# Performance work log

Measured on AMD Instinct MI355X. Metric: run time of the kernel, lower is better.

Reference implementation:

```python
import jax, jax.numpy as jnp
import numpy as np

NUM = 8          # group_heads
ALPHA = 1000.0   # Pos_Enc alpha
BETA = 100.0     # Pos_Enc beta


def setup_inputs() -> dict:
    key = jax.random.key(0)
    ks = jax.random.split(key, 19)
    N, C, H = 16384, 64, 1024
    gs1 = H // NUM
    s = 0.02
    r = lambda k, shp: jax.random.normal(k, shp, dtype=jnp.float32) * s
    return {
        "features": jax.random.normal(ks[0], (N, C), dtype=jnp.float32),
        "fc1_w": r(ks[1], (C, H)), "fc1_b": r(ks[2], (H,)),
        "fc2_w": r(ks[3], (H, C)), "fc2_b": r(ks[4], (C,)),
        "g1_w": r(ks[5], (H, H)), "g1_b": r(ks[6], (H,)),
        "g2_w": r(ks[7], (H, H)), "g2_b": r(ks[8], (H,)),
        "gg1_w": r(ks[9], (gs1, gs1)), "gg1_b": r(ks[10], (gs1,)),
        "gg2_w": r(ks[11], (gs1, gs1)), "gg2_b": r(ks[12], (gs1,)),
        "wq": r(ks[13], (H, H)), "wk": r(ks[14], (H, H)), "wv": r(ks[15], (H, H)),
        "wq2": r(ks[16], (gs1, gs1)), "wk2": r(ks[17], (gs1, gs1)),
        "lpe": jax.random.normal(ks[18], (1,), dtype=jnp.float32) * 0.1,
    }


def _mlp(x, w1, b1, w2, b2):
    return jax.nn.relu(x @ w1 + b1) @ w2 + b2


def reference(features, fc1_w, fc1_b, fc2_w, fc2_b, g1_w, g1_b, g2_w, g2_b,
              gg1_w, gg1_b, gg2_w, gg2_b, wq, wk, wv, wq2, wk2, lpe):
    N, C = features.shape
    H = fc1_w.shape[1]
    gs1 = H // NUM   # feature-group size
    gs2 = N // NUM   # token-group size

    x = features @ fc1_w + fc1_b                      # (N, H)

    # --- attn1: per-feature-group vector attention (shared weights -> vectorized)
    xg = x.reshape(N, NUM, gs1)                       # contiguous feature slices
    q1 = xg @ wq2
    k1 = xg @ wk2
    h1 = _mlp(q1 - k1, gg1_w, gg1_b, gg2_w, gg2_b)
    attn1 = jax.nn.softmax(h1 / np.sqrt(gs1).astype(np.float32), axis=0)
    attn1 = attn1.reshape(N, H)                       # concat over groups = reshape

    # --- attn2: source bug: loop uses stale i=NUM-1, so the LAST token group
    # is processed NUM times and tiled along tokens.
    gf2 = x[(NUM - 1) * gs2:, :]                      # (gs2, H)
    q2 = gf2 @ wq
    k2 = gf2 @ wk
    h2 = _mlp(q2 - k2, g1_w, g1_b, g2_w, g2_b)
    a2 = jax.nn.softmax(h2 / np.sqrt(H).astype(np.float32), axis=0)
    attn2 = jnp.tile(a2, (NUM, 1))                    # (N, H)

    attn = attn1 + attn2
    v = x @ wv                                        # (N, H)

    # --- sinusoidal positional encoding (Pos_Enc), only coord-0 slice survives
    xyz = features[:, :3]                             # (N, 3)
    feat_dim = H // 2
    feat_range = jnp.arange(feat_dim, dtype=jnp.float32)
    dim_embed = jnp.power(jnp.float32(ALPHA), feat_range / feat_dim)
    div = BETA * xyz[..., None] / dim_embed           # (N, 3, feat_dim)
    emb = jnp.concatenate([jnp.sin(div), jnp.cos(div)], axis=-1)  # (N, 3, H)
    pe = (emb + lpe[0]) * lpe[0]
    pe0 = pe[:, 0, :]                                 # (N, H) first coordinate

    res = attn * (v + pe0)                            # elementwise einsum bmf,bmf->bmf
    out = res @ fc2_w + fc2_b + features              # residual
    return out
```

## Files before the change

### kernel.cpp

```cpp
#include <hip/hip_runtime.h>
#include <hip/hip_bf16.h>
#include <math.h>
#include <type_traits>


typedef __attribute__((ext_vector_type(8))) short short8;
typedef __attribute__((ext_vector_type(4))) float f32x4;
typedef __attribute__((ext_vector_type(4))) float float4v;

#define GLOAD_LDS16(gptr, lptr)                                                 \
    __builtin_amdgcn_global_load_lds(                                           \
        (const __attribute__((address_space(1))) void*)(gptr),                  \
        (__attribute__((address_space(3))) void*)(lptr), 16, 0, 0)

static __device__ __forceinline__ unsigned short f2bf_bits(float v) {
    __hip_bfloat16 h = __float2bfloat16(v);
    return __builtin_bit_cast(unsigned short, h);
}
static __device__ __forceinline__ float bf_bits2f(unsigned short u) {
    return __bfloat162float(__builtin_bit_cast(__hip_bfloat16, u));
}
static __device__ __forceinline__ int swz16(int r, int c16) {
    return (r << 4) + (c16 ^ (r & 7));
}
static __device__ __forceinline__ int swz_elem(int r, int c) {
    return (r << 7) + ((((c << 1) ^ ((r & 7) << 4))) >> 1);
}
static __device__ __forceinline__ int xcd_swz(int bid, int nwg) {
    return (bid & 7) * (nwg >> 3) + (bid >> 3);
}

static __device__ void conv_t_dev(const float* __restrict__ A, const float* __restrict__ Bsub,
                                  __hip_bfloat16* __restrict__ Ot, int K, int N,
                                  int bx, int by, int tid, float* t )
{
    const int n0 = bx * 32, k0 = by * 128;
    const int tx = tid & 31, ty = tid >> 5;
    const int ksub = (K - k0 < 128) ? (K - k0) / 32 : 4;
    for (int s = 0; s < ksub; ++s) {
        const int kk = k0 + s * 32;
        #pragma unroll
        for (int j = 0; j < 4; ++j) {
            int k = kk + ty + j * 8;
            float v = A[(long)k * N + n0 + tx];
            if (Bsub) v -= Bsub[(long)k * N + n0 + tx];
            t[(ty + j * 8) * 33 + tx] = v;
        }
        __syncthreads();
        #pragma unroll
        for (int j = 0; j < 4; ++j) {
            int n = n0 + ty + j * 8;
            Ot[(long)n * K + kk + tx] = __float2bfloat16(t[tx * 33 + ty + j * 8]);
        }
        __syncthreads();
    }
}

__global__ __launch_bounds__(256) void prep_k(
    const float* __restrict__ features, const float* __restrict__ fc2_w,
    const float* __restrict__ fc2_b, const float* __restrict__ g1_w,
    const float* __restrict__ g2_w, const float* __restrict__ wq,
    const float* __restrict__ wk, const float* __restrict__ wv,
    const float* __restrict__ wq2, const float* __restrict__ wk2,
    const float* __restrict__ gg1_w, const float* __restrict__ gg2_w,
    __hip_bfloat16* __restrict__ fc2T, __hip_bfloat16* __restrict__ wdT,
    __hip_bfloat16* __restrict__ wvT, __hip_bfloat16* __restrict__ g1T,
    __hip_bfloat16* __restrict__ g2T, __hip_bfloat16* __restrict__ wd2T,
    __hip_bfloat16* __restrict__ gg1T, __hip_bfloat16* __restrict__ gg2T,
    float* __restrict__ invde, float* __restrict__ out)
{
    __shared__ float t[32 * 33];
    const int bid = blockIdx.x;
    const int tid = threadIdx.x;

    if (bid == 0) {
        #pragma unroll
        for (int i = 0; i < 2; ++i) {
            int idx = tid + i * 256;
            invde[idx] = exp2f(-9.96578428466209f * (float)idx * (1.f / 512.f));
        }
    } else if (bid < 257) {
        const float4v* f4 = (const float4v*)features;
        float4v* o4 = (float4v*)out;
        const float4v* b4 = (const float4v*)fc2_b;
        long base = (long)(bid - 1) * 1024;
        #pragma unroll
        for (int i = 0; i < 4; ++i) {
            long idx = base + tid + i * 256;
            o4[idx] = f4[idx] + b4[idx & 15];
        }
    } else if (bid < 513) {
        int tt = bid - 257;  conv_t_dev(wq, wk, wdT, 1024, 1024, tt & 31, tt >> 5, tid, t);
    } else if (bid < 769) {
        int tt = bid - 513;  conv_t_dev(wv, nullptr, wvT, 1024, 1024, tt & 31, tt >> 5, tid, t);
    } else if (bid < 1025) {
        int tt = bid - 769;  conv_t_dev(g1_w, nullptr, g1T, 1024, 1024, tt & 31, tt >> 5, tid, t);
    } else if (bid < 1281) {
        int tt = bid - 1025; conv_t_dev(g2_w, nullptr, g2T, 1024, 1024, tt & 31, tt >> 5, tid, t);
    } else if (bid < 1297) {
        int tt = bid - 1281; conv_t_dev(fc2_w, nullptr, fc2T, 1024, 64, tt & 1, tt >> 1, tid, t);
    } else if (bid < 1301) {
        int tt = bid - 1297; conv_t_dev(wq2, wk2, wd2T, 128, 128, tt & 3, 0, tid, t);
    } else if (bid < 1305) {
        int tt = bid - 1301; conv_t_dev(gg1_w, nullptr, gg1T, 128, 128, tt & 3, 0, tid, t);
    } else {
        int tt = bid - 1305; conv_t_dev(gg2_w, nullptr, gg2T, 128, 128, tt & 3, 0, tid, t);
    }
}

__global__ __launch_bounds__(256) void xgemm_k(
    const float* __restrict__ features, const float* __restrict__ fc1_w,
    const float* __restrict__ fc1_b, __hip_bfloat16* __restrict__ xb)
{
    __shared__ __align__(16) char smem[32768];
    unsigned short* As = (unsigned short*)smem;
    unsigned short* Bs = (unsigned short*)(smem + 16384);
    const int tile = blockIdx.x;
    const int tid = threadIdx.x;
    const int bm = (tile >> 3) << 7, bn = (tile & 7) << 7;
    const int wid = tid >> 6, lane = tid & 63;
    const int wm = (wid >> 1) << 6, wn = (wid & 1) << 6;
    const int l15 = lane & 15, kg = lane >> 4;

    #pragma unroll
    for (int i = 0; i < 8; ++i) {
        int idx = i * 256 + tid;
        int r = idx >> 4, c4 = idx & 15;
        float4v f = *(const float4v*)(features + (long)(bm + r) * 64 + c4 * 4);
        unsigned int p0 = f2bf_bits(f[0]) | ((unsigned int)f2bf_bits(f[1]) << 16);
        unsigned int p1 = f2bf_bits(f[2]) | ((unsigned int)f2bf_bits(f[3]) << 16);
        int dst = r * 64 + (((c4 >> 1) ^ (r & 7)) << 3) + (c4 & 1) * 4;
        unsigned int* p = (unsigned int*)&As[dst];
        p[0] = p0; p[1] = p1;
    }
    #pragma unroll
    for (int i = 0; i < 8; ++i) {
        int idx = i * 256 + tid;
        int k = idx >> 5, c4b = idx & 31;
        float4v g = *(const float4v*)(fc1_w + (long)k * 1024 + bn + c4b * 4);
        #pragma unroll
        for (int q = 0; q < 4; ++q) {
            int n = c4b * 4 + q;
            Bs[n * 64 + (((k >> 3) ^ (n & 7)) << 3) + (k & 7)] = f2bf_bits(g[q]);
        }
    }
    __syncthreads();

    f32x4 acc[4][4] = {};
    #pragma unroll
    for (int ks2 = 0; ks2 < 2; ++ks2) {
        const int kslot = ks2 * 4 + kg;
        short8 af[4], bf_[4];
        #pragma unroll
        for (int m = 0; m < 4; ++m) {
            int r = wm + m * 16 + l15;
            af[m] = *(const short8*)&As[r * 64 + ((kslot ^ (r & 7)) << 3)];
        }
        #pragma unroll
        for (int n = 0; n < 4; ++n) {
            int r = wn + n * 16 + l15;
            bf_[n] = *(const short8*)&Bs[r * 64 + ((kslot ^ (r & 7)) << 3)];
        }
        #pragma unroll
        for (int m = 0; m < 4; ++m)
            #pragma unroll
            for (int n = 0; n < 4; ++n)
                acc[m][n] = __builtin_amdgcn_mfma_f32_16x16x32_bf16(
                    af[m], bf_[n], acc[m][n], 0, 0, 0);
    }
    const int rq = kg << 2;
    #pragma unroll
    for (int n = 0; n < 4; ++n) {
        const int col = bn + wn + n * 16 + l15;
        const float bv = fc1_b[col];
        #pragma unroll
        for (int m = 0; m < 4; ++m)
            #pragma unroll
            for (int j = 0; j < 4; ++j)
                xb[(long)(bm + wm + m * 16 + rq + j) * 1024 + col] =
                    __float2bfloat16(acc[m][n][j] + bv);
    }
}

template <int OP, bool CS>
static __device__ void gemm6464_dev(
    const __hip_bfloat16* __restrict__ A, const __hip_bfloat16* __restrict__ Bt,
    const float* __restrict__ bias, __hip_bfloat16* __restrict__ Co,
    float scale, float* __restrict__ pcs, int swz, int tid, char* smem)
{
    const int wid = tid >> 6, lane = tid & 63;
    const int bm = (swz >> 4) << 6, bn = (swz & 15) << 6;
    const int wm = (wid >> 1) << 5, wn = (wid & 1) << 5;
    f32x4 acc[2][2] = {};
    const int l15 = lane & 15, kg = lane >> 4;
    const int rS = tid >> 2;
    const int c4s = (tid & 3) ^ ((rS >> 1) & 3);

#define G66_STAGE(b, k0)                                                        \
    { char* base = smem + (b) * 8192;                                           \
      GLOAD_LDS16(A + (long)(bm + rS) * 1024 + (k0) + c4s * 8,                  \
                  base + (wid << 6) * 16);                                      \
      GLOAD_LDS16(Bt + (long)(bn + rS) * 1024 + (k0) + c4s * 8,                 \
                  base + 4096 + (wid << 6) * 16); }

    G66_STAGE(0, 0);
    #pragma unroll 2
    for (int kt = 0; kt < 32; ++kt) {
        if (kt < 31) {
            G66_STAGE((kt + 1) & 1, (kt + 1) * 32);
            asm volatile("s_waitcnt vmcnt(2)" ::: "memory");
        } else {
            asm volatile("s_waitcnt vmcnt(0)" ::: "memory");
        }
        __builtin_amdgcn_s_barrier();
        __builtin_amdgcn_sched_barrier(0);
        const char* AsB = smem + (kt & 1) * 8192;
        const char* BsB = AsB + 4096;
        short8 af[2], bf_[2];
        #pragma unroll
        for (int m = 0; m < 2; ++m) {
            const int R = wm + m * 16 + l15;
            af[m] = *(const short8*)(AsB + R * 64 + ((kg ^ ((R >> 1) & 3)) << 4));
        }
        #pragma unroll
        for (int n = 0; n < 2; ++n) {
            const int R = wn + n * 16 + l15;
            bf_[n] = *(const short8*)(BsB + R * 64 + ((kg ^ ((R >> 1) & 3)) << 4));
        }
        __builtin_amdgcn_s_setprio(1);
        #pragma unroll
        for (int m = 0; m < 2; ++m)
            #pragma unroll
            for (int n = 0; n < 2; ++n)
                acc[m][n] = __builtin_amdgcn_mfma_f32_16x16x32_bf16(
                    af[m], bf_[n], acc[m][n], 0, 0, 0);
        __builtin_amdgcn_s_setprio(0);
        __builtin_amdgcn_s_barrier();
    }
#undef G66_STAGE

    const int rq = kg << 2;
    float csum[2];
    #pragma unroll
    for (int n = 0; n < 2; ++n) {
        const int col = bn + wn + n * 16 + l15;
        const float bv = bias ? bias[col] : 0.f;
        csum[n] = 0.f;
        #pragma unroll
        for (int m = 0; m < 2; ++m) {
            #pragma unroll
            for (int j = 0; j < 4; ++j) {
                const int row = bm + wm + m * 16 + rq + j;
                float cv = acc[m][n][j] + bv;
                if (OP == 1) cv = fmaxf(cv, 0.f);
                if (OP == 2) cv = __expf(cv * scale);
                if (CS) csum[n] += cv;
                Co[(long)row * 1024 + col] = __float2bfloat16(cv);
            }
        }
    }
    if (CS) {
        __syncthreads();
        float* ps = (float*)smem;
        const int slot = ((wid >> 1) << 2) | kg;
        #pragma unroll
        for (int n = 0; n < 2; ++n)
            ps[(wn + n * 16 + l15) * 8 + slot] = csum[n];
        __syncthreads();
        if (tid < 64) {
            float s = 0.f;
            #pragma unroll
            for (int q = 0; q < 8; ++q) s += ps[tid * 8 + q];
            pcs[(long)(swz >> 4) * 1024 + bn + tid] = s;
        }
    }
}

__global__ __launch_bounds__(256) void t1_k(
    const __hip_bfloat16* __restrict__ A, const __hip_bfloat16* __restrict__ Bt,
    __hip_bfloat16* __restrict__ Co)
{
    __shared__ __align__(16) char smem[16384];
    const int swz = xcd_swz(blockIdx.y * gridDim.x + blockIdx.x, gridDim.x * gridDim.y);
    gemm6464_dev<0, false>(A, Bt, nullptr, Co, 0.f, nullptr, swz, threadIdx.x, smem);
}
__global__ __launch_bounds__(256) void t2_k(
    const __hip_bfloat16* __restrict__ A, const __hip_bfloat16* __restrict__ Bt,
    const float* __restrict__ bias, __hip_bfloat16* __restrict__ Co)
{
    __shared__ __align__(16) char smem[16384];
    const int swz = xcd_swz(blockIdx.y * gridDim.x + blockIdx.x, gridDim.x * gridDim.y);
    gemm6464_dev<1, false>(A, Bt, bias, Co, 0.f, nullptr, swz, threadIdx.x, smem);
}
__global__ __launch_bounds__(256) void t3_k(
    const __hip_bfloat16* __restrict__ A, const __hip_bfloat16* __restrict__ Bt,
    const float* __restrict__ bias, __hip_bfloat16* __restrict__ Co,
    float* __restrict__ pcs)
{
    __shared__ __align__(16) char smem[16384];
    const int swz = xcd_swz(blockIdx.y * gridDim.x + blockIdx.x, gridDim.x * gridDim.y);
    gemm6464_dev<2, true>(A, Bt, bias, Co, 0.03125f, pcs, swz, threadIdx.x, smem);
}

__global__ __launch_bounds__(256) void chain_k(
    const __hip_bfloat16* __restrict__ xb,
    const __hip_bfloat16* __restrict__ w1T,
    const __hip_bfloat16* __restrict__ w2T,
    const __hip_bfloat16* __restrict__ w3T,
    const float* __restrict__ b2, const float* __restrict__ b3,
    __hip_bfloat16* __restrict__ e1, float* __restrict__ pcs1)
{
    __shared__ __align__(16) char smem[65536];
    unsigned short* act = (unsigned short*)smem;
    unsigned short* Wb  = (unsigned short*)(smem + 32768);
    const int tid = threadIdx.x;
    const int wid = tid >> 6, lane = tid & 63;
    const int wm = (wid >> 1) << 6, wn = (wid & 1) << 6;
    const int tileIdx = blockIdx.x;
    const long tile = (long)tileIdx * (128 * 128);

    #pragma unroll
    for (int i = 0; i < 8; ++i) {
        int L = i * 256 + wid * 64 + lane;
        int r = L >> 4, c16o = (L & 15) ^ (r & 7);
        GLOAD_LDS16(xb + tile + r * 128 + c16o * 8,
                    (char*)act + (i * 256 + wid * 64) * 16);
        GLOAD_LDS16(w1T + r * 128 + c16o * 8,
                    (char*)Wb + (i * 256 + wid * 64) * 16);
    }
    __syncthreads();

    f32x4 acc[4][4];
    const int rq = (lane >> 4) << 2;

#define CHAIN_ZERO()                                                            \
    _Pragma("unroll") for (int m = 0; m < 4; ++m)                               \
        _Pragma("unroll") for (int n = 0; n < 4; ++n)                           \
            acc[m][n] = (f32x4){0.f, 0.f, 0.f, 0.f};

#define CHAIN_MM()                                                              \
    _Pragma("unroll") for (int ks = 0; ks < 4; ++ks) {                          \
        short8 af[4], bfv[4];                                                   \
        const int kc = ks * 4 + (lane >> 4);                                    \
        _Pragma("unroll") for (int m = 0; m < 4; ++m) {                         \
            int r = wm + m * 16 + (lane & 15);                                  \
            af[m] = *(const short8*)((const char*)act + swz16(r, kc) * 16);     \
        }                                                                       \
        _Pragma("unroll") for (int n = 0; n < 4; ++n) {                         \
            int r = wn + n * 16 + (lane & 15);                                  \
            bfv[n] = *(const short8*)((const char*)Wb + swz16(r, kc) * 16);     \
        }                                                                       \
        _Pragma("unroll") for (int m = 0; m < 4; ++m)                           \
            _Pragma("unroll") for (int n = 0; n < 4; ++n)                       \
                acc[m][n] = __builtin_amdgcn_mfma_f32_16x16x32_bf16(            \
                    af[m], bfv[n], acc[m][n], 0, 0, 0);                         \
    }

#define STAGE_W(wptr)                                                           \
    _Pragma("unroll") for (int i = 0; i < 8; ++i) {                             \
        int L = i * 256 + wid * 64 + lane;                                      \
        int r = L >> 4, c16o = (L & 15) ^ (r & 7);                              \
        GLOAD_LDS16((wptr) + r * 128 + c16o * 8,                                \
                    (char*)Wb + (i * 256 + wid * 64) * 16);                     \
    }

    CHAIN_ZERO(); CHAIN_MM();
    __syncthreads();
    STAGE_W(w2T);
    #pragma unroll
    for (int m = 0; m < 4; ++m)
        #pragma unroll
        for (int n = 0; n < 4; ++n)
            #pragma unroll
            for (int j = 0; j < 4; ++j) {
                int row = wm + m * 16 + rq + j, col = wn + n * 16 + (lane & 15);
                act[swz_elem(row, col)] = f2bf_bits(acc[m][n][j]);
            }
    __syncthreads();

    CHAIN_ZERO(); CHAIN_MM();
    __syncthreads();
    STAGE_W(w3T);
    {
        float bv[4];
        #pragma unroll
        for (int n = 0; n < 4; ++n) bv[n] = b2[wn + n * 16 + (lane & 15)];
        #pragma unroll
        for (int m = 0; m < 4; ++m)
            #pragma unroll
            for (int n = 0; n < 4; ++n)
                #pragma unroll
                for (int j = 0; j < 4; ++j) {
                    int row = wm + m * 16 + rq + j, col = wn + n * 16 + (lane & 15);
                    act[swz_elem(row, col)] = f2bf_bits(fmaxf(acc[m][n][j] + bv[n], 0.f));
                }
    }
    __syncthreads();

    CHAIN_ZERO(); CHAIN_MM();
    __syncthreads();
    {
        float bv[4];
        #pragma unroll
        for (int n = 0; n < 4; ++n) bv[n] = b3[wn + n * 16 + (lane & 15)];
        #pragma unroll
        for (int m = 0; m < 4; ++m)
            #pragma unroll
            for (int n = 0; n < 4; ++n)
                #pragma unroll
                for (int j = 0; j < 4; ++j) {
                    int row = wm + m * 16 + rq + j, col = wn + n * 16 + (lane & 15);
                    float ev = __expf((acc[m][n][j] + bv[n]) * 0.08838834764831845f);
                    act[swz_elem(row, col)] = f2bf_bits(ev);
                }
    }
    __syncthreads();

    #pragma unroll
    for (int i = 0; i < 8; ++i) {
        int idx = i * 256 + tid;
        int r = idx >> 4, c16o = idx & 15;
        short8 vd = *(const short8*)((const char*)act + swz16(r, c16o) * 16);
        *(short8*)((__hip_bfloat16*)e1 + tile + r * 128 + c16o * 8) = vd;
    }
    #pragma unroll
    for (int i = 0; i < 4; ++i) {
        int p = i * 256 + tid;
        int g = p >> 7, c = p & 127;
        float s = 0.f;
        #pragma unroll
        for (int t16 = 0; t16 < 16; ++t16) {
            int r = t16 * 8 + g;
            s += bf_bits2f(act[swz_elem(r, c)]);
        }
        pcs1[(long)tileIdx * 1024 + p] = s;
    }
#undef CHAIN_ZERO
#undef CHAIN_MM
#undef STAGE_W
}

__global__ __launch_bounds__(1024) void reduce_k(
    const float* __restrict__ pcs1, const float* __restrict__ pcs2,
    float* __restrict__ rcs1, float* __restrict__ rcs2)
{
    __shared__ float red[16][64];
    const int tx = threadIdx.x, ty = threadIdx.y;
    if (blockIdx.x < 16) {
        const int col = blockIdx.x * 64 + tx;
        float s = 0.f;
        for (int p = ty; p < 1024; p += 16) s += pcs1[(long)p * 1024 + col];
        red[ty][tx] = s;
        __syncthreads();
        if (ty == 0) {
            float t = 0.f;
            #pragma unroll
            for (int q = 0; q < 16; ++q) t += red[q][tx];
            rcs1[col] = 1.f / t;
        }
    } else {
        const int col = (blockIdx.x - 16) * 64 + tx;
        float s = 0.f;
        for (int p = ty; p < 32; p += 16) s += pcs2[(long)p * 1024 + col];
        red[ty][tx] = s;
        __syncthreads();
        if (ty == 0) {
            float t = 0.f;
            #pragma unroll
            for (int q = 0; q < 16; ++q) t += red[q][tx];
            rcs2[col] = 1.f / t;
        }
    }
}

__global__ __launch_bounds__(256) void vres_k(
    const __hip_bfloat16* __restrict__ A, const __hip_bfloat16* __restrict__ Bt,
    const __hip_bfloat16* __restrict__ e1, const __hip_bfloat16* __restrict__ e2,
    const float* __restrict__ rcs1, const float* __restrict__ rcs2,
    const float* __restrict__ invde, const float* __restrict__ feats,
    const float* __restrict__ lpe, const __hip_bfloat16* __restrict__ fc2T,
    float* __restrict__ out)
{
    __shared__ __align__(16) char smem[65536];
    unsigned short* st = (unsigned short*)smem;

    const int tid = threadIdx.x;
    const int wid = tid >> 6;
    const int lane = tid & 63;
    const int swz = xcd_swz(blockIdx.y * gridDim.x + blockIdx.x, gridDim.x * gridDim.y);
    const int bm = (swz >> 3) << 7, bn = (swz & 7) << 7;
    const int wm = (wid >> 1) << 6, wn = (wid & 1) << 6;

    f32x4 acc[4][4] = {};
    const int c8 = tid & 7;
    const int l15 = lane & 15;
    const int kg = lane >> 4;
    const int arow = wm + l15;
    const int brow = wn + l15;

#define VR_STAGE(b, k0)                                                         \
    { char* base = smem + (b) * 32768;                                          \
      _Pragma("unroll") for (int i = 0; i < 4; ++i) {                           \
        const int r = i * 32 + (tid >> 3);                                      \
        const int c8s = c8 ^ (r & 7);                                           \
        GLOAD_LDS16(A + (long)(bm + r) * 1024 + (k0) + c8s * 8,                 \
                    base + (i * 256 + wid * 64) * 16);                          \
        GLOAD_LDS16(Bt + (long)(bn + r) * 1024 + (k0) + c8s * 8,                \
                    base + 16384 + (i * 256 + wid * 64) * 16); } }

    VR_STAGE(0, 0);
    #pragma unroll 2
    for (int kt = 0; kt < 16; ++kt) {
        if (kt < 15) {
            VR_STAGE((kt + 1) & 1, (kt + 1) * 64);
            asm volatile("s_waitcnt vmcnt(8)" ::: "memory");
        } else {
            asm volatile("s_waitcnt vmcnt(0)" ::: "memory");
        }
        __builtin_amdgcn_s_barrier();
        __builtin_amdgcn_sched_barrier(0);
        const __hip_bfloat16* As = (const __hip_bfloat16*)(smem + (kt & 1) * 32768);
        const __hip_bfloat16* Bs = (const __hip_bfloat16*)(smem + (kt & 1) * 32768 + 16384);
        __builtin_amdgcn_s_setprio(1);
        #pragma unroll
        for (int ks2 = 0; ks2 < 2; ++ks2) {
            const int kslot = ks2 * 4 + kg;
            short8 af[4], bf_[4];
            #pragma unroll
            for (int m = 0; m < 4; ++m) {
                const int r = arow + m * 16;
                af[m] = *(const short8*)(As + (r * 8 + (kslot ^ (r & 7))) * 8);
            }
            #pragma unroll
            for (int n = 0; n < 4; ++n) {
                const int r = brow + n * 16;
                bf_[n] = *(const short8*)(Bs + (r * 8 + (kslot ^ (r & 7))) * 8);
            }
            #pragma unroll
            for (int m = 0; m < 4; ++m)
                #pragma unroll
                for (int n = 0; n < 4; ++n)
                    acc[m][n] = __builtin_amdgcn_mfma_f32_16x16x32_bf16(
                        af[m], bf_[n], acc[m][n], 0, 0, 0);
        }
        __builtin_amdgcn_s_setprio(0);
        __builtin_amdgcn_s_barrier();
    }
#undef VR_STAGE

    const int rq = kg << 2;
    #pragma unroll
    for (int m = 0; m < 4; ++m)
        #pragma unroll
        for (int n = 0; n < 4; ++n)
            #pragma unroll
            for (int j = 0; j < 4; ++j)
                st[(wm + m * 16 + rq + j) * 136 + wn + n * 16 + l15] =
                    f2bf_bits(acc[m][n][j]);
    __syncthreads();

    const float lp = lpe[0];
    #pragma unroll
    for (int p = 0; p < 4; ++p) {
        const int r = p * 32 + (tid >> 3);
        const int cc = (tid & 7) << 4;
        const int grow = bm + r;
        const float angs = 100.f * feats[(long)grow * 64];
        const long goff = (long)grow * 1024 + bn + cc;
        const long goff2 = (long)(grow & 2047) * 1024 + bn + cc;
        short8 ev1[2], ev2[2], sv[2];
        ev1[0] = *(const short8*)((const unsigned short*)e1 + goff);
        ev1[1] = *(const short8*)((const unsigned short*)e1 + goff + 8);
        ev2[0] = *(const short8*)((const unsigned short*)e2 + goff2);
        ev2[1] = *(const short8*)((const unsigned short*)e2 + goff2 + 8);
        sv[0] = *(const short8*)&st[r * 136 + cc];
        sv[1] = *(const short8*)&st[r * 136 + cc + 8];
        unsigned short ov[16];
        #pragma unroll
        for (int q = 0; q < 16; ++q) {
            const int h = bn + cc + q;
            const float ang = angs * invde[h & 511];
            const float tr = (h < 512) ? __sinf(ang) : __cosf(ang);
            const float a = bf_bits2f((unsigned short)ev1[q >> 3][q & 7]) * rcs1[h] +
                            bf_bits2f((unsigned short)ev2[q >> 3][q & 7]) * rcs2[h];
            const float vv = bf_bits2f((unsigned short)sv[q >> 3][q & 7]);
            ov[q] = f2bf_bits(a * (vv + (tr + lp) * lp));
        }
        *(short8*)&st[r * 136 + cc] = *(short8*)&ov[0];
        *(short8*)&st[r * 136 + cc + 8] = *(short8*)&ov[8];
    }
    __syncthreads();

    {
        const int wmO = wid << 5;
        f32x4 aco[2][4] = {};
        #pragma unroll
        for (int ks = 0; ks < 4; ++ks) {
            short8 afo[2], bfo[4];
            #pragma unroll
            for (int m = 0; m < 2; ++m)
                afo[m] = *(const short8*)&st[(wmO + m * 16 + l15) * 136 + ks * 32 + kg * 8];
            #pragma unroll
            for (int n = 0; n < 4; ++n)
                bfo[n] = *(const short8*)((const unsigned short*)fc2T +
                                          (long)(n * 16 + l15) * 1024 + bn + ks * 32 + kg * 8);
            #pragma unroll
            for (int m = 0; m < 2; ++m)
                #pragma unroll
                for (int n = 0; n < 4; ++n)
                    aco[m][n] = __builtin_amdgcn_mfma_f32_16x16x32_bf16(
                        afo[m], bfo[n], aco[m][n], 0, 0, 0);
        }
        #pragma unroll
        for (int m = 0; m < 2; ++m)
            #pragma unroll
            for (int n = 0; n < 4; ++n)
                #pragma unroll
                for (int j = 0; j < 4; ++j) {
                    const int row = bm + wmO + m * 16 + rq + j;
                    atomicAdd(&out[(long)row * 64 + n * 16 + l15], aco[m][n][j]);
                }
    }
}

extern "C" void kernel_launch(void* const* d_in, const int* in_sizes, int n_in,
                              void* d_out, int out_size, void* d_ws, size_t ws_size,
                              hipStream_t stream) {
    const float* features = (const float*)d_in[0];
    const float* fc1_w = (const float*)d_in[1];
    const float* fc1_b = (const float*)d_in[2];
    const float* fc2_w = (const float*)d_in[3];
    const float* fc2_b = (const float*)d_in[4];
    const float* g1_w = (const float*)d_in[5];
    const float* g1_b = (const float*)d_in[6];
    const float* g2_w = (const float*)d_in[7];
    const float* g2_b = (const float*)d_in[8];
    const float* gg1_w = (const float*)d_in[9];
    const float* gg1_b = (const float*)d_in[10];
    const float* gg2_w = (const float*)d_in[11];
    const float* gg2_b = (const float*)d_in[12];
    const float* wq = (const float*)d_in[13];
    const float* wk = (const float*)d_in[14];
    const float* wv = (const float*)d_in[15];
    const float* wq2 = (const float*)d_in[16];
    const float* wk2 = (const float*)d_in[17];
    const float* lpe = (const float*)d_in[18];
    float* out = (float*)d_out;

    char* ws = (char*)d_ws;
    const size_t MB = 1024ull * 1024ull;
    __hip_bfloat16* xb   = (__hip_bfloat16*)ws;
    __hip_bfloat16* e1   = (__hip_bfloat16*)(ws + 32 * MB);
    __hip_bfloat16* d2b  = (__hip_bfloat16*)(ws + 64 * MB);
    __hip_bfloat16* t2b  = (__hip_bfloat16*)(ws + 68 * MB);
    __hip_bfloat16* e2b  = (__hip_bfloat16*)(ws + 72 * MB);
    float*          pcs1 = (float*)(ws + 76 * MB);
    float*          pcs2 = (float*)(ws + 80 * MB);
    char* W = ws + 81 * MB;
    __hip_bfloat16* wdT   = (__hip_bfloat16*)W;
    __hip_bfloat16* wvT   = (__hip_bfloat16*)(W + 2 * MB);
    __hip_bfloat16* g1T   = (__hip_bfloat16*)(W + 4 * MB);
    __hip_bfloat16* g2T   = (__hip_bfloat16*)(W + 6 * MB);
    __hip_bfloat16* fc2T  = (__hip_bfloat16*)(W + 8 * MB);
    __hip_bfloat16* wd2T  = (__hip_bfloat16*)(W + 8 * MB + 256 * 1024);
    __hip_bfloat16* gg1T  = (__hip_bfloat16*)(W + 8 * MB + 320 * 1024);
    __hip_bfloat16* gg2T  = (__hip_bfloat16*)(W + 8 * MB + 384 * 1024);
    float* rcs1  = (float*)(W + 9 * MB);
    float* rcs2  = rcs1 + 1024;
    float* invde = rcs2 + 1024;

    prep_k<<<1309, 256, 0, stream>>>(
        features, fc2_w, fc2_b, g1_w, g2_w, wq, wk, wv, wq2, wk2,
        gg1_w, gg2_w, fc2T, wdT, wvT, g1T, g2T, wd2T, gg1T, gg2T, invde, out);

    xgemm_k<<<1024, 256, 0, stream>>>(features, fc1_w, fc1_b, xb);

    t1_k<<<dim3(16, 32), 256, 0, stream>>>(xb + (size_t)14336 * 1024, wdT, d2b);

    chain_k<<<1024, 256, 0, stream>>>(xb, wd2T, gg1T, gg2T, gg1_b, gg2_b, e1, pcs1);

    t2_k<<<dim3(16, 32), 256, 0, stream>>>(d2b, g1T, g1_b, t2b);
    t3_k<<<dim3(16, 32), 256, 0, stream>>>(t2b, g2T, g2_b, e2b, pcs2);

    reduce_k<<<32, dim3(64, 16), 0, stream>>>(pcs1, pcs2, rcs1, rcs2);

    vres_k<<<dim3(8, 128), 256, 0, stream>>>(
        xb, wvT, e1, e2b, rcs1, rcs2, invde, features, lpe, fc2T, out);
}
```

Before: 289.9 us.

## Triple-buffer 64x64 GEMM loads and double vres_k warps to 512 threads

The shared 64x64 GEMM used by t1/t2/t3 moves from double to triple buffering, prefetching two k-tiles ahead and waiting with a looser vmcnt so more global loads stay in flight. Its LDS allocation grows accordingly. Separately, vres_k is relaunched with 512 threads (8 waves), each wave owning a smaller 64x32 accumulator tile, and the epilogue and fc2 projection are re-partitioned so each wave handles 16 rows. This raises latency hiding and occupancy per block at the cost of more LDS per GEMM block and a changed register and LDS-sharing profile in vres_k.

```diff
diff --git a/kernel.cpp b/kernel.cpp
--- a/kernel.cpp
+++ b/kernel.cpp
@@ -204,17 +204,20 @@
                   base + 4096 + (wid << 6) * 16); }
 
     G66_STAGE(0, 0);
-    #pragma unroll 2
+    G66_STAGE(1, 32);
+    int cur = 0, nxt = 2;
     for (int kt = 0; kt < 32; ++kt) {
-        if (kt < 31) {
-            G66_STAGE((kt + 1) & 1, (kt + 1) * 32);
+        if (kt < 30) {
+            G66_STAGE(nxt, (kt + 2) * 32);
+            asm volatile("s_waitcnt vmcnt(4)" ::: "memory");
+        } else if (kt == 30) {
             asm volatile("s_waitcnt vmcnt(2)" ::: "memory");
         } else {
             asm volatile("s_waitcnt vmcnt(0)" ::: "memory");
         }
         __builtin_amdgcn_s_barrier();
         __builtin_amdgcn_sched_barrier(0);
-        const char* AsB = smem + (kt & 1) * 8192;
+        const char* AsB = smem + cur * 8192;
         const char* BsB = AsB + 4096;
         short8 af[2], bf_[2];
         #pragma unroll
@@ -236,6 +239,8 @@
                     af[m], bf_[n], acc[m][n], 0, 0, 0);
         __builtin_amdgcn_s_setprio(0);
         __builtin_amdgcn_s_barrier();
+        cur = (cur == 2) ? 0 : cur + 1;
+        nxt = (nxt == 2) ? 0 : nxt + 1;
     }
 #undef G66_STAGE
 
@@ -280,7 +285,7 @@
     const __hip_bfloat16* __restrict__ A, const __hip_bfloat16* __restrict__ Bt,
     __hip_bfloat16* __restrict__ Co)
 {
-    __shared__ __align__(16) char smem[16384];
+    __shared__ __align__(16) char smem[24576];
     const int swz = xcd_swz(blockIdx.y * gridDim.x + blockIdx.x, gridDim.x * gridDim.y);
     gemm6464_dev<0, false>(A, Bt, nullptr, Co, 0.f, nullptr, swz, threadIdx.x, smem);
 }
@@ -288,7 +293,7 @@
     const __hip_bfloat16* __restrict__ A, const __hip_bfloat16* __restrict__ Bt,
     const float* __restrict__ bias, __hip_bfloat16* __restrict__ Co)
 {
-    __shared__ __align__(16) char smem[16384];
+    __shared__ __align__(16) char smem[24576];
     const int swz = xcd_swz(blockIdx.y * gridDim.x + blockIdx.x, gridDim.x * gridDim.y);
     gemm6464_dev<1, false>(A, Bt, bias, Co, 0.f, nullptr, swz, threadIdx.x, smem);
 }
@@ -297,7 +302,7 @@
     const float* __restrict__ bias, __hip_bfloat16* __restrict__ Co,
     float* __restrict__ pcs)
 {
-    __shared__ __align__(16) char smem[16384];
+    __shared__ __align__(16) char smem[24576];
     const int swz = xcd_swz(blockIdx.y * gridDim.x + blockIdx.x, gridDim.x * gridDim.y);
     gemm6464_dev<2, true>(A, Bt, bias, Co, 0.03125f, pcs, swz, threadIdx.x, smem);
 }
@@ -473,7 +478,7 @@
     }
 }
 
-__global__ __launch_bounds__(256) void vres_k(
+__global__ __launch_bounds__(512, 4) void vres_k(
     const __hip_bfloat16* __restrict__ A, const __hip_bfloat16* __restrict__ Bt,
     const __hip_bfloat16* __restrict__ e1, const __hip_bfloat16* __restrict__ e2,
     const float* __restrict__ rcs1, const float* __restrict__ rcs2,
@@ -489,10 +494,10 @@
     const int lane = tid & 63;
     const int swz = xcd_swz(blockIdx.y * gridDim.x + blockIdx.x, gridDim.x * gridDim.y);
     const int bm = (swz >> 3) << 7, bn = (swz & 7) << 7;
-    const int wm = (wid >> 1) << 6, wn = (wid & 1) << 6;
-
-    f32x4 acc[4][4] = {};
-    const int c8 = tid & 7;
+    const int wm = (wid >> 2) << 6;
+    const int wn = (wid & 3) << 5;
+
+    f32x4 acc[4][2] = {};
     const int l15 = lane & 15;
     const int kg = lane >> 4;
     const int arow = wm + l15;
@@ -500,20 +505,21 @@
 
 #define VR_STAGE(b, k0)                                                         \
     { char* base = smem + (b) * 32768;                                          \
-      _Pragma("unroll") for (int i = 0; i < 4; ++i) {                           \
-        const int r = i * 32 + (tid >> 3);                                      \
-        const int c8s = c8 ^ (r & 7);                                           \
+      _Pragma("unroll") for (int i = 0; i < 2; ++i) {                           \
+        const int idx = i * 512 + tid;                                          \
+        const int r = idx >> 3;                                                 \
+        const int c8s = (idx & 7) ^ (r & 7);                                    \
         GLOAD_LDS16(A + (long)(bm + r) * 1024 + (k0) + c8s * 8,                 \
-                    base + (i * 256 + wid * 64) * 16);                          \
+                    base + (i * 512 + wid * 64) * 16);                          \
         GLOAD_LDS16(Bt + (long)(bn + r) * 1024 + (k0) + c8s * 8,                \
-                    base + 16384 + (i * 256 + wid * 64) * 16); } }
+                    base + 16384 + (i * 512 + wid * 64) * 16); } }
 
     VR_STAGE(0, 0);
     #pragma unroll 2
     for (int kt = 0; kt < 16; ++kt) {
         if (kt < 15) {
             VR_STAGE((kt + 1) & 1, (kt + 1) * 64);
-            asm volatile("s_waitcnt vmcnt(8)" ::: "memory");
+            asm volatile("s_waitcnt vmcnt(4)" ::: "memory");
         } else {
             asm volatile("s_waitcnt vmcnt(0)" ::: "memory");
         }
@@ -525,21 +531,21 @@
         #pragma unroll
         for (int ks2 = 0; ks2 < 2; ++ks2) {
             const int kslot = ks2 * 4 + kg;
-            short8 af[4], bf_[4];
+            short8 af[4], bf_[2];
             #pragma unroll
             for (int m = 0; m < 4; ++m) {
                 const int r = arow + m * 16;
                 af[m] = *(const short8*)(As + (r * 8 + (kslot ^ (r & 7))) * 8);
             }
             #pragma unroll
-            for (int n = 0; n < 4; ++n) {
+            for (int n = 0; n < 2; ++n) {
                 const int r = brow + n * 16;
                 bf_[n] = *(const short8*)(Bs + (r * 8 + (kslot ^ (r & 7))) * 8);
             }
             #pragma unroll
             for (int m = 0; m < 4; ++m)
                 #pragma unroll
-                for (int n = 0; n < 4; ++n)
+                for (int n = 0; n < 2; ++n)
                     acc[m][n] = __builtin_amdgcn_mfma_f32_16x16x32_bf16(
                         af[m], bf_[n], acc[m][n], 0, 0, 0);
         }
@@ -552,7 +558,7 @@
     #pragma unroll
     for (int m = 0; m < 4; ++m)
         #pragma unroll
-        for (int n = 0; n < 4; ++n)
+        for (int n = 0; n < 2; ++n)
             #pragma unroll
             for (int j = 0; j < 4; ++j)
                 st[(wm + m * 16 + rq + j) * 136 + wn + n * 16 + l15] =
@@ -561,8 +567,8 @@
 
     const float lp = lpe[0];
     #pragma unroll
-    for (int p = 0; p < 4; ++p) {
-        const int r = p * 32 + (tid >> 3);
+    for (int p = 0; p < 2; ++p) {
+        const int r = p * 64 + (tid >> 3);
         const int cc = (tid & 7) << 4;
         const int grow = bm + r;
         const float angs = 100.f * feats[(long)grow * 64];
@@ -592,34 +598,25 @@
     __syncthreads();
 
     {
-        const int wmO = wid << 5;
-        f32x4 aco[2][4] = {};
+        const int wmO = wid << 4;
+        f32x4 aco[4] = {};
         #pragma unroll
         for (int ks = 0; ks < 4; ++ks) {
-            short8 afo[2], bfo[4];
-            #pragma unroll
-            for (int m = 0; m < 2; ++m)
-                afo[m] = *(const short8*)&st[(wmO + m * 16 + l15) * 136 + ks * 32 + kg * 8];
-            #pragma unroll
-            for (int n = 0; n < 4; ++n)
-                bfo[n] = *(const short8*)((const unsigned short*)fc2T +
-                                          (long)(n * 16 + l15) * 1024 + bn + ks * 32 + kg * 8);
-            #pragma unroll
-            for (int m = 0; m < 2; ++m)
-                #pragma unroll
-                for (int n = 0; n < 4; ++n)
-                    aco[m][n] = __builtin_amdgcn_mfma_f32_16x16x32_bf16(
-                        afo[m], bfo[n], aco[m][n], 0, 0, 0);
-        }
-        #pragma unroll
-        for (int m = 0; m < 2; ++m)
-            #pragma unroll
-            for (int n = 0; n < 4; ++n)
-                #pragma unroll
-                for (int j = 0; j < 4; ++j) {
-                    const int row = bm + wmO + m * 16 + rq + j;
-                    atomicAdd(&out[(long)row * 64 + n * 16 + l15], aco[m][n][j]);
-                }
+            short8 afo = *(const short8*)&st[(wmO + l15) * 136 + ks * 32 + kg * 8];
+            #pragma unroll
+            for (int n = 0; n < 4; ++n) {
+                short8 bfo = *(const short8*)((const unsigned short*)fc2T +
+                                              (long)(n * 16 + l15) * 1024 + bn + ks * 32 + kg * 8);
+                aco[n] = __builtin_amdgcn_mfma_f32_16x16x32_bf16(afo, bfo, aco[n], 0, 0, 0);
+            }
+        }
+        #pragma unroll
+        for (int n = 0; n < 4; ++n)
+            #pragma unroll
+            for (int j = 0; j < 4; ++j) {
+                const int row = bm + wmO + rq + j;
+                atomicAdd(&out[(long)row * 64 + n * 16 + l15], aco[n][j]);
+            }
     }
 }
 
@@ -684,6 +681,6 @@
 
     reduce_k<<<32, dim3(64, 16), 0, stream>>>(pcs1, pcs2, rcs1, rcs2);
 
-    vres_k<<<dim3(8, 128), 256, 0, stream>>>(
+    vres_k<<<dim3(8, 128), 512, 0, stream>>>(
         xb, wvT, e1, e2b, rcs1, rcs2, invde, features, lpe, fc2T, out);
 }
```

New measurement: 286.8 us. About the same (-1.1%).
